# Performance work log

Measured on AMD Instinct MI355X. Metric: run time of the kernel, lower is better.

Reference implementation:

```python
import jax, jax.numpy as jnp
import numpy as np

CHUNK_SIZE = 2048
EPS = 1e-12  # torch F.normalize clamps the norm at 1e-12


def _l2_normalize(x, axis):
    n = jnp.sqrt(jnp.sum(x * x, axis=axis, keepdims=True))
    return x / jnp.maximum(n, EPS)


def _nnfm_loss(F_r, F_s, chunk_size=CHUNK_SIZE):
    B, C, H_r, W_r = F_r.shape
    _, _, H_s, W_s = F_s.shape
    N_r = H_r * W_r
    N_s = H_s * W_s
    assert N_r % chunk_size == 0, "N_r must be divisible by chunk_size for this reference"
    n_chunks = N_r // chunk_size

    F_s_norm = _l2_normalize(F_s.reshape(B, C, N_s), axis=1)  # (B, C, N_s)
    F_r_flat = F_r.reshape(B, C, N_r)
    # (n_chunks, B, C, chunk) -- contiguous chunks along N_r, matching the torch loop
    chunks = F_r_flat.reshape(B, C, n_chunks, chunk_size).transpose(2, 0, 1, 3)

    def body(chunk):  # chunk: (B, C, chunk_size)
        cn = _l2_normalize(chunk, axis=1)
        sim = jnp.einsum('bcn,bcm->bnm', cn, F_s_norm)  # (B, chunk, N_s)
        # min(1 - sim) over N_s == 1 - max(sim)
        return 1.0 - jnp.max(sim, axis=2)  # (B, chunk)

    min_dists = jax.lax.map(body, chunks)  # (n_chunks, B, chunk) -- bounded memory
    return jnp.mean(min_dists)


def setup_inputs() -> dict:
    key = jax.random.key(0)
    k1, k2 = jax.random.split(key)
    F_r = jax.random.normal(k1, (1, 768, 128, 128), dtype=jnp.float32)
    F_s = jax.random.normal(k2, (1, 768, 128, 128), dtype=jnp.float32)
    return {"F_r": F_r, "F_s": F_s}


def reference(F_r, F_s):
    return _nnfm_loss(F_r, F_s)
```

## Files before the change

kernel.cpp:

```cpp
#include <hip/hip_runtime.h>
#include <cstdint>
#include <cstddef>

#define C_DIM 768
#define N_DIM 16384

typedef __attribute__((ext_vector_type(8))) short short8;
typedef __attribute__((ext_vector_type(4))) float f32x4;

__device__ __forceinline__ ushort f2bf(float f) {
    uint32_t u = __float_as_uint(f);
    uint32_t r = 0x7fffu + ((u >> 16) & 1u);
    return (ushort)((u + r) >> 16);
}

__device__ __forceinline__ void async_ld16(const void* g, void* l) {
    __builtin_amdgcn_global_load_lds(
        (__attribute__((address_space(1))) void*)g,
        (__attribute__((address_space(3))) void*)l,
        16, 0, 0);
}

__global__ __launch_bounds__(256) void norm_tr(const float* __restrict__ F0,
                                               ushort* __restrict__ T0,
                                               const float* __restrict__ F1,
                                               ushort* __restrict__ T1) {
    const float*  F = blockIdx.y ? F1 : F0;
    ushort*       T = blockIdx.y ? T1 : T0;
    const int i0 = blockIdx.x * 64;
    const int t  = threadIdx.x;
    const int tx = t & 63;
    const int ty = t >> 6;

    float ss = 0.f;
    for (int c = ty; c < C_DIM; c += 4) {
        float v = F[(size_t)c * N_DIM + i0 + tx];
        ss += v * v;
    }
    __shared__ float red[4][64];
    __shared__ float scale[64];
    red[ty][tx] = ss;
    __syncthreads();
    if (t < 64) {
        float s = red[0][t] + red[1][t] + red[2][t] + red[3][t];
        float n = sqrtf(s);
        scale[t] = 1.0f / fmaxf(n, 1e-12f);
    }
    __syncthreads();

    __shared__ float tile[64][65];
    const int i_l   = t >> 3;
    const int c_off = (t & 7) * 8;
    for (int c0 = 0; c0 < C_DIM; c0 += 64) {
        #pragma unroll
        for (int rr = 0; rr < 16; ++rr) {
            int c_l = rr * 4 + ty;
            tile[c_l][tx] = F[(size_t)(c0 + c_l) * N_DIM + i0 + tx] * scale[tx];
        }
        __syncthreads();
        #pragma unroll
        for (int half = 0; half < 2; ++half) {
            int il = i_l + half * 32;
            __align__(16) ushort pack[8];
            #pragma unroll
            for (int j = 0; j < 8; ++j)
                pack[j] = f2bf(tile[c_off + j][il]);
            *(uint4*)&T[(size_t)(i0 + il) * C_DIM + c0 + c_off] = *(const uint4*)pack;
        }
        __syncthreads();
    }
}

__global__ __launch_bounds__(512) void gemm_rowmax(const ushort* __restrict__ A,
                                                   const ushort* __restrict__ B,
                                                   unsigned* __restrict__ rowkey) {
    __shared__ __align__(16) ushort As[2][128 * 32];
    __shared__ __align__(16) ushort Bs[2][256 * 32];

    const int t    = threadIdx.x;
    const int lane = t & 63;
    const int w    = t >> 6;
    const int wm   = w >> 2;
    const int wn   = w & 3;

    const int bid   = blockIdx.x;
    const int xcd   = bid & 7;
    const int local = bid >> 3;
    const int m0    = (local >> 3) * 128;
    const int n0    = (xcd * 8 + (local & 7)) * 256;

    f32x4 acc[4][4];
    #pragma unroll
    for (int i = 0; i < 4; ++i)
        #pragma unroll
        for (int j = 0; j < 4; ++j)
            acc[i][j] = (f32x4){0.f, 0.f, 0.f, 0.f};

    const int kq = ((t & 3) ^ ((t >> 3) & 3)) * 8;
    const ushort* ag  = A + (size_t)(m0 + (t >> 2)) * C_DIM + kq;
    const ushort* bg0 = B + (size_t)(n0 + (t >> 2)) * C_DIM + kq;
    const ushort* bg1 = bg0 + (size_t)128 * C_DIM;
    const int lda = t * 8;
    const int ldb0 = t * 8, ldb1 = 128 * 32 + t * 8;

    const int qp    = ((lane >> 4) ^ ((lane >> 1) & 3)) * 8;
    const int a_off = (wm * 64 + (lane & 15)) * 32 + qp;
    const int b_off = (wn * 64 + (lane & 15)) * 32 + qp;

    async_ld16(ag,  As[0] + lda);
    async_ld16(bg0, Bs[0] + ldb0);
    async_ld16(bg1, Bs[0] + ldb1);

    int buf = 0;
    for (int k0 = 0; k0 < C_DIM; k0 += 32) {
        __syncthreads();
        if (k0 + 32 < C_DIM) {
            const int kn = k0 + 32, nb = buf ^ 1;
            async_ld16(ag + kn,  As[nb] + lda);
            async_ld16(bg0 + kn, Bs[nb] + ldb0);
            async_ld16(bg1 + kn, Bs[nb] + ldb1);
        }

        const ushort* Ab = As[buf];
        const ushort* Bb = Bs[buf];
        short8 af[4], bfr[4];
        #pragma unroll
        for (int mt = 0; mt < 4; ++mt)
            af[mt] = *(const short8*)(Ab + a_off + mt * 16 * 32);
        #pragma unroll
        for (int nt = 0; nt < 4; ++nt)
            bfr[nt] = *(const short8*)(Bb + b_off + nt * 16 * 32);
        #pragma unroll
        for (int mt = 0; mt < 4; ++mt)
            #pragma unroll
            for (int nt = 0; nt < 4; ++nt)
                acc[mt][nt] = __builtin_amdgcn_mfma_f32_16x16x32_bf16(
                    af[mt], bfr[nt], acc[mt][nt], 0, 0, 0);
        buf ^= 1;
    }

    #pragma unroll
    for (int mt = 0; mt < 4; ++mt) {
        #pragma unroll
        for (int reg = 0; reg < 4; ++reg) {
            float v = fmaxf(fmaxf(acc[mt][0][reg], acc[mt][1][reg]),
                            fmaxf(acc[mt][2][reg], acc[mt][3][reg]));
            #pragma unroll
            for (int off = 1; off < 16; off <<= 1)
                v = fmaxf(v, __shfl_xor(v, off, 64));
            if ((lane & 15) == 0) {
                int m = m0 + wm * 64 + mt * 16 + (lane >> 4) * 4 + reg;
                unsigned u = __float_as_uint(v);
                u = (u & 0x80000000u) ? ~u : (u | 0x80000000u);
                atomicMax(&rowkey[m], u);
            }
        }
    }
}

__global__ __launch_bounds__(1024) void finalize(const unsigned* __restrict__ rowkey,
                                                 float* __restrict__ out) {
    const int t = threadIdx.x;
    float s = 0.f;
    for (int i = t; i < N_DIM; i += 1024) {
        unsigned u = rowkey[i];
        float f = (u & 0x80000000u) ? __uint_as_float(u ^ 0x80000000u)
                                    : __uint_as_float(~u);
        s += f;
    }
    #pragma unroll
    for (int off = 32; off >= 1; off >>= 1)
        s += __shfl_down(s, off, 64);
    __shared__ float part[16];
    if ((t & 63) == 0) part[t >> 6] = s;
    __syncthreads();
    if (t == 0) {
        float tot = 0.f;
        #pragma unroll
        for (int i = 0; i < 16; ++i) tot += part[i];
        out[0] = 1.0f - tot * (1.0f / (float)N_DIM);
    }
}

extern "C" void kernel_launch(void* const* d_in, const int* in_sizes, int n_in,
                              void* d_out, int out_size, void* d_ws, size_t ws_size,
                              hipStream_t stream) {
    const float* F_r = (const float*)d_in[0];
    const float* F_s = (const float*)d_in[1];

    ushort*   Rt     = (ushort*)d_ws;
    ushort*   St     = Rt + (size_t)N_DIM * C_DIM;
    unsigned* rowkey = (unsigned*)(St + (size_t)N_DIM * C_DIM);
    float*    out    = (float*)d_out;

    hipLaunchKernelGGL(norm_tr, dim3(N_DIM / 64, 2), dim3(256), 0, stream,
                       F_r, Rt, F_s, St);
    hipMemsetAsync(rowkey, 0, N_DIM * sizeof(unsigned), stream);
    hipLaunchKernelGGL(gemm_rowmax, dim3((N_DIM / 128) * (N_DIM / 256)), dim3(512),
                       0, stream, Rt, St, rowkey);
    hipLaunchKernelGGL(finalize, dim3(1), dim3(1024), 0, stream, rowkey, out);
}
```

Before: 692.0 us.

## Quantize normalized features to int8 and use i8 MFMA for similarity GEMM

Replaces the bf16 normalized-transpose with per-row absmax int8 quantization, storing a combined dequant/normalization scale per row. The GEMM uses the 16x16x64 i8 MFMA with 64-wide K tiles, which halves operand bytes and doubles the math rate relative to bf16. The row max is computed after applying the column scale, and the row scale is applied at the end. Int8 quantization adds error to the similarity maxima, so accuracy relative to the fp32 reference is at risk.

```diff
diff --git a/kernel.cpp b/kernel.cpp
--- a/kernel.cpp
+++ b/kernel.cpp
@@ -5,14 +5,7 @@
 #define C_DIM 768
 #define N_DIM 16384
 
-typedef __attribute__((ext_vector_type(8))) short short8;
-typedef __attribute__((ext_vector_type(4))) float f32x4;
-
-__device__ __forceinline__ ushort f2bf(float f) {
-    uint32_t u = __float_as_uint(f);
-    uint32_t r = 0x7fffu + ((u >> 16) & 1u);
-    return (ushort)((u + r) >> 16);
-}
+typedef __attribute__((ext_vector_type(4))) int i32x4;
 
 __device__ __forceinline__ void async_ld16(const void* g, void* l) {
     __builtin_amdgcn_global_load_lds(
@@ -21,30 +14,39 @@
         16, 0, 0);
 }
 
-__global__ __launch_bounds__(256) void norm_tr(const float* __restrict__ F0,
-                                               ushort* __restrict__ T0,
-                                               const float* __restrict__ F1,
-                                               ushort* __restrict__ T1) {
+__global__ __launch_bounds__(256) void norm_q(const float* __restrict__ F0,
+                                              signed char* __restrict__ Q0,
+                                              float* __restrict__ S0,
+                                              const float* __restrict__ F1,
+                                              signed char* __restrict__ Q1,
+                                              float* __restrict__ S1) {
     const float*  F = blockIdx.y ? F1 : F0;
-    ushort*       T = blockIdx.y ? T1 : T0;
+    signed char*  Q = blockIdx.y ? Q1 : Q0;
+    float*        S = blockIdx.y ? S1 : S0;
     const int i0 = blockIdx.x * 64;
     const int t  = threadIdx.x;
     const int tx = t & 63;
     const int ty = t >> 6;
 
-    float ss = 0.f;
+    float ss = 0.f, mx = 0.f;
     for (int c = ty; c < C_DIM; c += 4) {
         float v = F[(size_t)c * N_DIM + i0 + tx];
         ss += v * v;
-    }
-    __shared__ float red[4][64];
-    __shared__ float scale[64];
-    red[ty][tx] = ss;
+        mx = fmaxf(mx, fabsf(v));
+    }
+    __shared__ float red_s[4][64];
+    __shared__ float red_m[4][64];
+    __shared__ float qscale[64];
+    red_s[ty][tx] = ss;
+    red_m[ty][tx] = mx;
     __syncthreads();
     if (t < 64) {
-        float s = red[0][t] + red[1][t] + red[2][t] + red[3][t];
-        float n = sqrtf(s);
-        scale[t] = 1.0f / fmaxf(n, 1e-12f);
+        float s = red_s[0][t] + red_s[1][t] + red_s[2][t] + red_s[3][t];
+        float m = fmaxf(fmaxf(red_m[0][t], red_m[1][t]),
+                        fmaxf(red_m[2][t], red_m[3][t]));
+        float n = fmaxf(sqrtf(s), 1e-12f);
+        qscale[t] = 127.0f / m;
+        S[i0 + t] = m / (127.0f * n);
     }
     __syncthreads();
 
@@ -55,27 +57,37 @@
         #pragma unroll
         for (int rr = 0; rr < 16; ++rr) {
             int c_l = rr * 4 + ty;
-            tile[c_l][tx] = F[(size_t)(c0 + c_l) * N_DIM + i0 + tx] * scale[tx];
+            tile[c_l][tx] = F[(size_t)(c0 + c_l) * N_DIM + i0 + tx] * qscale[tx];
         }
         __syncthreads();
         #pragma unroll
         for (int half = 0; half < 2; ++half) {
             int il = i_l + half * 32;
-            __align__(16) ushort pack[8];
-            #pragma unroll
-            for (int j = 0; j < 8; ++j)
-                pack[j] = f2bf(tile[c_off + j][il]);
-            *(uint4*)&T[(size_t)(i0 + il) * C_DIM + c0 + c_off] = *(const uint4*)pack;
+            unsigned lo = 0, hi = 0;
+            #pragma unroll
+            for (int j = 0; j < 4; ++j) {
+                int q = __float2int_rn(tile[c_off + j][il]);
+                lo |= (unsigned)(q & 0xff) << (8 * j);
+            }
+            #pragma unroll
+            for (int j = 0; j < 4; ++j) {
+                int q = __float2int_rn(tile[c_off + 4 + j][il]);
+                hi |= (unsigned)(q & 0xff) << (8 * j);
+            }
+            uint2 u; u.x = lo; u.y = hi;
+            *(uint2*)&Q[(size_t)(i0 + il) * C_DIM + c0 + c_off] = u;
         }
         __syncthreads();
     }
 }
 
-__global__ __launch_bounds__(512) void gemm_rowmax(const ushort* __restrict__ A,
-                                                   const ushort* __restrict__ B,
+__global__ __launch_bounds__(512) void gemm_rowmax(const signed char* __restrict__ A,
+                                                   const signed char* __restrict__ B,
+                                                   const float* __restrict__ sA,
+                                                   const float* __restrict__ sB,
                                                    unsigned* __restrict__ rowkey) {
-    __shared__ __align__(16) ushort As[2][128 * 32];
-    __shared__ __align__(16) ushort Bs[2][256 * 32];
+    __shared__ __align__(16) signed char As[2][128 * 64];
+    __shared__ __align__(16) signed char Bs[2][256 * 64];
 
     const int t    = threadIdx.x;
     const int lane = t & 63;
@@ -89,67 +101,75 @@
     const int m0    = (local >> 3) * 128;
     const int n0    = (xcd * 8 + (local & 7)) * 256;
 
-    f32x4 acc[4][4];
+    i32x4 acc[4][4];
     #pragma unroll
     for (int i = 0; i < 4; ++i)
         #pragma unroll
         for (int j = 0; j < 4; ++j)
-            acc[i][j] = (f32x4){0.f, 0.f, 0.f, 0.f};
-
-    const int kq = ((t & 3) ^ ((t >> 3) & 3)) * 8;
-    const ushort* ag  = A + (size_t)(m0 + (t >> 2)) * C_DIM + kq;
-    const ushort* bg0 = B + (size_t)(n0 + (t >> 2)) * C_DIM + kq;
-    const ushort* bg1 = bg0 + (size_t)128 * C_DIM;
-    const int lda = t * 8;
-    const int ldb0 = t * 8, ldb1 = 128 * 32 + t * 8;
-
-    const int qp    = ((lane >> 4) ^ ((lane >> 1) & 3)) * 8;
-    const int a_off = (wm * 64 + (lane & 15)) * 32 + qp;
-    const int b_off = (wn * 64 + (lane & 15)) * 32 + qp;
+            acc[i][j] = (i32x4){0, 0, 0, 0};
+
+    const int kq = ((t & 3) ^ ((t >> 3) & 3)) * 16;
+    const signed char* ag  = A + (size_t)(m0 + (t >> 2)) * C_DIM + kq;
+    const signed char* bg0 = B + (size_t)(n0 + (t >> 2)) * C_DIM + kq;
+    const signed char* bg1 = bg0 + (size_t)128 * C_DIM;
+    const int lda  = t * 16;
+    const int ldb0 = t * 16, ldb1 = 128 * 64 + t * 16;
+
+    const int qp    = ((lane >> 4) ^ ((lane >> 1) & 3)) * 16;
+    const int a_off = (wm * 64 + (lane & 15)) * 64 + qp;
+    const int b_off = (wn * 64 + (lane & 15)) * 64 + qp;
 
     async_ld16(ag,  As[0] + lda);
     async_ld16(bg0, Bs[0] + ldb0);
     async_ld16(bg1, Bs[0] + ldb1);
 
     int buf = 0;
-    for (int k0 = 0; k0 < C_DIM; k0 += 32) {
+    for (int k0 = 0; k0 < C_DIM; k0 += 64) {
         __syncthreads();
-        if (k0 + 32 < C_DIM) {
-            const int kn = k0 + 32, nb = buf ^ 1;
+        if (k0 + 64 < C_DIM) {
+            const int kn = k0 + 64, nb = buf ^ 1;
             async_ld16(ag + kn,  As[nb] + lda);
             async_ld16(bg0 + kn, Bs[nb] + ldb0);
             async_ld16(bg1 + kn, Bs[nb] + ldb1);
         }
 
-        const ushort* Ab = As[buf];
-        const ushort* Bb = Bs[buf];
-        short8 af[4], bfr[4];
+        const signed char* Ab = As[buf];
+        const signed char* Bb = Bs[buf];
+        i32x4 af[4], bfr[4];
         #pragma unroll
         for (int mt = 0; mt < 4; ++mt)
-            af[mt] = *(const short8*)(Ab + a_off + mt * 16 * 32);
+            af[mt] = *(const i32x4*)(Ab + a_off + mt * 16 * 64);
         #pragma unroll
         for (int nt = 0; nt < 4; ++nt)
-            bfr[nt] = *(const short8*)(Bb + b_off + nt * 16 * 32);
+            bfr[nt] = *(const i32x4*)(Bb + b_off + nt * 16 * 64);
         #pragma unroll
         for (int mt = 0; mt < 4; ++mt)
             #pragma unroll
             for (int nt = 0; nt < 4; ++nt)
-                acc[mt][nt] = __builtin_amdgcn_mfma_f32_16x16x32_bf16(
+                acc[mt][nt] = __builtin_amdgcn_mfma_i32_16x16x64_i8(
                     af[mt], bfr[nt], acc[mt][nt], 0, 0, 0);
         buf ^= 1;
     }
 
+    float sb[4];
+    #pragma unroll
+    for (int nt = 0; nt < 4; ++nt)
+        sb[nt] = sB[n0 + wn * 64 + nt * 16 + (lane & 15)];
+
     #pragma unroll
     for (int mt = 0; mt < 4; ++mt) {
         #pragma unroll
         for (int reg = 0; reg < 4; ++reg) {
-            float v = fmaxf(fmaxf(acc[mt][0][reg], acc[mt][1][reg]),
-                            fmaxf(acc[mt][2][reg], acc[mt][3][reg]));
+            float v = fmaxf(fmaxf((float)acc[mt][0][reg] * sb[0],
+                                  (float)acc[mt][1][reg] * sb[1]),
+                            fmaxf((float)acc[mt][2][reg] * sb[2],
+                                  (float)acc[mt][3][reg] * sb[3]));
             #pragma unroll
             for (int off = 1; off < 16; off <<= 1)
                 v = fmaxf(v, __shfl_xor(v, off, 64));
             if ((lane & 15) == 0) {
                 int m = m0 + wm * 64 + mt * 16 + (lane >> 4) * 4 + reg;
+                v *= sA[m];
                 unsigned u = __float_as_uint(v);
                 u = (u & 0x80000000u) ? ~u : (u | 0x80000000u);
                 atomicMax(&rowkey[m], u);
@@ -188,15 +208,17 @@
     const float* F_r = (const float*)d_in[0];
     const float* F_s = (const float*)d_in[1];
 
-    ushort*   Rt     = (ushort*)d_ws;
-    ushort*   St     = Rt + (size_t)N_DIM * C_DIM;
-    unsigned* rowkey = (unsigned*)(St + (size_t)N_DIM * C_DIM);
-    float*    out    = (float*)d_out;
-
-    hipLaunchKernelGGL(norm_tr, dim3(N_DIM / 64, 2), dim3(256), 0, stream,
-                       F_r, Rt, F_s, St);
+    signed char* Rq = (signed char*)d_ws;
+    signed char* Sq = Rq + (size_t)N_DIM * C_DIM;
+    float* sR       = (float*)(Sq + (size_t)N_DIM * C_DIM);
+    float* sS       = sR + N_DIM;
+    unsigned* rowkey= (unsigned*)(sS + N_DIM);
+    float* out      = (float*)d_out;
+
+    hipLaunchKernelGGL(norm_q, dim3(N_DIM / 64, 2), dim3(256), 0, stream,
+                       F_r, Rq, sR, F_s, Sq, sS);
     hipMemsetAsync(rowkey, 0, N_DIM * sizeof(unsigned), stream);
     hipLaunchKernelGGL(gemm_rowmax, dim3((N_DIM / 128) * (N_DIM / 256)), dim3(512),
-                       0, stream, Rt, St, rowkey);
+                       0, stream, Rq, Sq, sR, sS, rowkey);
     hipLaunchKernelGGL(finalize, dim3(1), dim3(1024), 0, stream, rowkey, out);
 }
```

New measurement: 714.1 us. +3.2%, slower.
